# Kernel optimization log

Measured on AMD Instinct MI355X. Metric: run time of the kernel, lower is better.

The kernel has to match this reference:

```python
import jax, jax.numpy as jnp
import numpy as np

B, D, C_IN = 2, 64, 4
N1, N2, N3, N4 = 32, 64, 96, 128
MQ, K = 1024, 5
DN = ('NCDHW', 'OIDHW', 'NCDHW')
PAD = [(2, 2)] * 3  # centered 5^3 kernel, matches Minkowski offsets in [-2, 2]


def setup_inputs() -> dict:
    rng = np.random.default_rng(0)
    mask = rng.random((B, D, D, D)) < 0.2
    x_feat = (rng.standard_normal((B, C_IN, D, D, D)) * mask[:, None]).astype(np.float32)
    Q_F = rng.random((B, MQ, 2)).astype(np.float32)  # per-point quality features (2 channels)

    def conv(cin, cout):
        w = (rng.standard_normal((cout, cin, K, K, K)) / np.sqrt(cin * K ** 3)).astype(np.float32)
        b = (0.01 * rng.standard_normal(cout)).astype(np.float32)
        return w, b

    def gdn(c):
        beta = np.ones(c, np.float32)
        gamma = (1e-4 * rng.random((c, c, K, K, K))).astype(np.float32)
        gamma[np.arange(c), np.arange(c), K // 2, K // 2, K // 2] += 0.1
        return beta, gamma

    w1, b1 = conv(C_IN, N1)
    w2, b2 = conv(N1, N2)
    w3, b3 = conv(N2, N3)
    w4, b4 = conv(N3, N4)
    beta1, gamma1 = gdn(N1)
    beta2, gamma2 = gdn(N2)
    beta3, gamma3 = gdn(N3)
    out = dict(x_feat=x_feat, mask=mask, Q_F=Q_F,
               w1=w1, b1=b1, w2=w2, b2=b2, w3=w3, b3=b3, w4=w4, b4=b4,
               beta1=beta1, gamma1=gamma1, beta2=beta2, gamma2=gamma2,
               beta3=beta3, gamma3=gamma3)
    return {k: jnp.asarray(v) for k, v in out.items()}


def _conv3d(x, w, b, stride):
    y = jax.lax.conv_general_dilated(x, w, (stride,) * 3, PAD, dimension_numbers=DN)
    return y + b[None, :, None, None, None]


def _pool_mask(m):
    # Minkowski stride-2 output coords = any occupied input in each 2x2x2 cell
    b, d = m.shape[0], m.shape[1]
    return m.reshape(b, d // 2, 2, d // 2, 2, d // 2, 2).max(axis=(2, 4, 6))


def _gdn(x, beta, gamma, scale, m):
    # conditional GDN: y = x / sqrt(beta + conv5(gamma, x^2)), scaled per batch by q[:,0]
    den = jax.lax.conv_general_dilated(x * x, gamma, (1, 1, 1), PAD, dimension_numbers=DN)
    y = x * jax.lax.rsqrt(beta[None, :, None, None, None] + den)
    return y * scale * m[:, None]


def reference(x_feat, mask, Q_F, w1, b1, w2, b2, w3, b3, w4, b4,
              beta1, gamma1, beta2, gamma2, beta3, gamma3):
    m0 = mask.astype(x_feat.dtype)
    q = jnp.mean(Q_F, axis=1)[None]                       # [1, B, 2]: per-batch mean of Q.F
    scale = q[0, :, 0][:, None, None, None, None]         # per-batch conditional scale

    c0 = m0.sum(axis=(1, 2, 3))                           # count_per_batch(x)
    m1 = _pool_mask(m0)
    x = _gdn(_conv3d(x_feat, w1, b1, 2) * m1[:, None], beta1, gamma1, scale, m1)
    c1 = m1.sum(axis=(1, 2, 3))
    m2 = _pool_mask(m1)
    x = _gdn(_conv3d(x, w2, b2, 2) * m2[:, None], beta2, gamma2, scale, m2)
    c2 = m2.sum(axis=(1, 2, 3))
    m3 = _pool_mask(m2)
    x = _gdn(_conv3d(x, w3, b3, 2) * m3[:, None], beta3, gamma3, scale, m3)
    x = _conv3d(x, w4, b4, 1) * m3[:, None]               # stride-1 conv keeps coords
    k = jnp.stack([c2, c1, c0]).astype(jnp.int32)         # k.reverse() in the original
    return x, q, k
```

## Files before the change

### kernel.cpp

```cpp
#include <hip/hip_runtime.h>
#include <math.h>

constexpr int Bn  = 2;
constexpr int CIN = 4;
constexpr int MQn = 1024;
constexpr int D0 = 64, D1 = 32, D2 = 16, D3 = 8;

constexpr int OUT_X = 0;
constexpr int OUT_Q = 131072;
constexpr int OUT_K = 131076;

constexpr size_t OFF_CNT   = 0;
constexpr size_t OFF_ZERO  = 8;
constexpr size_t OFF_D1    = 16;
constexpr size_t OFF_T2    = OFF_D1 + 2097152;
constexpr size_t OFF_D2    = OFF_T2 + 524288;
constexpr size_t OFF_T3    = OFF_D2 + 524288;
constexpr size_t OFF_D3    = OFF_T3 + 98304;
constexpr size_t ZERO_END  = OFF_D3 + 98304;
constexpr size_t OFF_SCALE = 3342360;
constexpr size_t OFF_M1    = 3342368;
constexpr size_t OFF_M2    = OFF_M1 + 65536;
constexpr size_t OFF_M3    = OFF_M2 + 8192;
constexpr size_t OFF_T1    = OFF_M3 + 1024;
constexpr size_t OFF_Y1    = OFF_T1 + 2097152;
constexpr size_t OFF_Y2    = OFF_Y1 + 2097152;
constexpr size_t OFF_SQ1   = OFF_Y2 + 524288;
constexpr size_t OFF_SQ2   = OFF_SQ1 + 1048576;
constexpr size_t OFF_SQ3   = OFF_SQ2 + 262144;
constexpr size_t OFF_Y3C   = OFF_SQ3 + 49152;
constexpr size_t OFF_W1T   = OFF_Y3C + 49152;
constexpr size_t OFF_W2T   = OFF_W1T + 16000;
constexpr size_t OFF_W3T   = OFF_W2T + 256000;
constexpr size_t OFF_WB1   = OFF_W3T + 768000;
constexpr size_t OFF_WB2   = OFF_WB1 + 64000;
constexpr size_t OFF_WB3   = OFF_WB2 + 256000;
constexpr size_t OFF_WB4   = OFF_WB3 + 576000;
constexpr size_t OFF_PU    = 12248736;
constexpr size_t OFF_Y1HL  = OFF_PU + 9437184;
constexpr size_t OFF_WB2S  = OFF_Y1HL + 3145728;
constexpr size_t OFF_WB1S  = OFF_WB2S + 384000;
constexpr size_t OFF_WB3S  = OFF_WB1S + 32000;
constexpr size_t OFF_Y2HL  = OFF_WB3S + 1152000;

typedef float v4f __attribute__((ext_vector_type(4)));
typedef __attribute__((ext_vector_type(8)))  short bf16x8v;
typedef __attribute__((ext_vector_type(4)))  short bf16x4v;
typedef __attribute__((ext_vector_type(16))) float f32x16v;

__device__ __forceinline__ void async_copy16(const float* g, float* l) {
    __builtin_amdgcn_global_load_lds(
        (const __attribute__((address_space(1))) void*)g,
        (__attribute__((address_space(3))) void*)l, 16, 0, 0);
}
__device__ __forceinline__ unsigned short f2bf(float f) {
    unsigned u = __float_as_uint(f);
    return (unsigned short)((u + 0x7FFFu + ((u >> 16) & 1u)) >> 16);
}
__device__ __forceinline__ float bf2f(unsigned short h) {
    return __uint_as_float((unsigned)h << 16);
}

__global__ void qmean_kernel(const float* __restrict__ QF, float* __restrict__ out_q,
                             float* __restrict__ scale) {
    int b = blockIdx.x >> 1, c = blockIdx.x & 1;
    float s = 0.f;
    for (int m = threadIdx.x; m < MQn; m += blockDim.x)
        s += QF[(b * MQn + m) * 2 + c];
    __shared__ float sh[256];
    sh[threadIdx.x] = s;
    __syncthreads();
    for (int st = 128; st > 0; st >>= 1) {
        if (threadIdx.x < st) sh[threadIdx.x] += sh[threadIdx.x + st];
        __syncthreads();
    }
    if (threadIdx.x == 0) {
        float mean = sh[0] / (float)MQn;
        out_q[b * 2 + c] = mean;
        if (c == 0) scale[b] = mean;
    }
}

__global__ void mask_pool1_kernel(const float* __restrict__ xf, float* __restrict__ m1,
                                  float* __restrict__ c0) {
    int idx = blockIdx.x * blockDim.x + threadIdx.x;
    int b = idx >> 15;
    int v = idx & 32767;
    int oz = v >> 10, oy = (v >> 5) & 31, ox = v & 31;
    float cnt = 0.f, mx = 0.f;
    for (int dz = 0; dz < 2; ++dz)
        for (int dy = 0; dy < 2; ++dy)
            for (int dx = 0; dx < 2; ++dx) {
                int z = 2 * oz + dz, y = 2 * oy + dy, x = 2 * ox + dx;
                size_t base = (size_t)b * CIN * D0 * D0 * D0 + ((size_t)z * D0 + y) * D0 + x;
                bool occ = false;
                for (int c = 0; c < CIN; ++c)
                    occ = occ || (xf[base + (size_t)c * D0 * D0 * D0] != 0.f);
                if (occ) { cnt += 1.f; mx = 1.f; }
            }
    m1[idx] = mx;
    __shared__ float sh[256];
    sh[threadIdx.x] = cnt;
    __syncthreads();
    for (int st = 128; st > 0; st >>= 1) {
        if (threadIdx.x < st) sh[threadIdx.x] += sh[threadIdx.x + st];
        __syncthreads();
    }
    if (threadIdx.x == 0) atomicAdd(&c0[b], sh[0]);
}

__global__ void pool_kernel(const float* __restrict__ min_, float* __restrict__ mout,
                            float* __restrict__ cacc, int Din) {
    int Do = Din >> 1;
    int per = Do * Do * Do;
    int idx = blockIdx.x * blockDim.x + threadIdx.x;
    int b = idx / per;
    int v = idx % per;
    int oz = v / (Do * Do), oy = (v / Do) % Do, ox = v % Do;
    float s = 0.f, mx = 0.f;
    for (int dz = 0; dz < 2; ++dz)
        for (int dy = 0; dy < 2; ++dy)
            for (int dx = 0; dx < 2; ++dx) {
                float val = min_[(((size_t)b * Din + 2 * oz + dz) * Din + 2 * oy + dy) * Din + 2 * ox + dx];
                s += val;
                mx = fmaxf(mx, val);
            }
    mout[idx] = mx;
    __shared__ float sh[256];
    sh[threadIdx.x] = s;
    __syncthreads();
    for (int st = 128; st > 0; st >>= 1) {
        if (threadIdx.x < st) sh[threadIdx.x] += sh[threadIdx.x + st];
        __syncthreads();
    }
    if (threadIdx.x == 0) atomicAdd(&cacc[b], sh[0]);
}

__global__ void writek_kernel(const float* __restrict__ cnt, float* __restrict__ outk) {
    int i = threadIdx.x;
    if (i < 6) {
        int row = i >> 1, b = i & 1;
        float v = (row == 0) ? cnt[4 + b] : (row == 1 ? cnt[2 + b] : cnt[b]);
        outk[i] = v;
    }
}

constexpr int MS1 = 0,        ME1 = 128000;
constexpr int MS2 = 128000,   ME2 = 640000;
constexpr int MS3 = 640000,   ME3 = 1792000;
constexpr int MS4 = 1792000,  ME4 = 3328000;
__global__ __launch_bounds__(256) void mwtrans_all_kernel(
        const float* __restrict__ g1, const float* __restrict__ g2,
        const float* __restrict__ g3, const float* __restrict__ w4,
        float* __restrict__ ws) {
    int idx = blockIdx.x * 256 + threadIdx.x;
    if (idx >= ME4) return;
    const float* src; unsigned short* dst; int nchn, cin, o;
    if (idx < ME1)      { src = g1; dst = (unsigned short*)(ws + OFF_WB1); nchn = 1; cin = 32; o = idx - MS1; }
    else if (idx < ME2) { src = g2; dst = (unsigned short*)(ws + OFF_WB2); nchn = 2; cin = 64; o = idx - MS2; }
    else if (idx < ME3) { src = g3; dst = (unsigned short*)(ws + OFF_WB3); nchn = 3; cin = 96; o = idx - MS3; }
    else                { src = w4; dst = (unsigned short*)(ws + OFF_WB4); nchn = 4; cin = 96; o = idx - MS4; }
    int j  = o & 7;
    int kc = (o >> 3) & 1;
    int n  = (o >> 4) & 31;
    int q  = o >> 9;
    int tap = q % 125;
    int q2  = q / 125;
    int nch = q2 % nchn;
    int cs  = q2 / nchn;
    int co = nch * 32 + n;
    int ci = cs * 16 + kc * 8 + j;
    dst[o] = f2bf(src[((size_t)co * cin + ci) * 125 + tap]);
}

constexpr int W2S_N = 768000;
__global__ __launch_bounds__(256) void w2s_kernel(const float* __restrict__ w2,
        unsigned short* __restrict__ dst) {
    int o = blockIdx.x * 256 + threadIdx.x;
    if (o >= W2S_N) return;
    int j = o & 7; int kc = (o >> 3) & 1; int n = (o >> 4) & 31; int q = o >> 9;
    int tap = q % 125; int q2 = q / 125; int c = q2 & 1; int cs = q2 >> 1;
    int co = c * 32 + n;
    int e = cs * 16 + kc * 8 + j;
    int ci = e & 31;
    float wv = w2[((size_t)co * 32 + ci) * 125 + tap];
    unsigned short h = f2bf(wv);
    if (e >= 64) h = f2bf(wv - bf2f(h));
    dst[o] = h;
}

constexpr int W3S_N = 2304000;
__global__ __launch_bounds__(256) void w3s_kernel(const float* __restrict__ w3,
        unsigned short* __restrict__ dst) {
    int o = blockIdx.x * 256 + threadIdx.x;
    if (o >= W3S_N) return;
    int j = o & 7; int kc = (o >> 3) & 1; int n = (o >> 4) & 31; int q = o >> 9;
    int tap = q % 125; int q2 = q / 125; int nch = q2 % 3; int cs = q2 / 3;
    int co = nch * 32 + n;
    int e = cs * 16 + kc * 8 + j;
    int ci = e & 63;
    float wv = w3[((size_t)co * 64 + ci) * 125 + tap];
    unsigned short h = f2bf(wv);
    if (e >= 128) h = f2bf(wv - bf2f(h));
    dst[o] = h;
}

constexpr int W1S_N = 64000;
__global__ __launch_bounds__(256) void w1s_kernel(const float* __restrict__ w1,
        unsigned short* __restrict__ dst) {
    int o = blockIdx.x * 256 + threadIdx.x;
    if (o >= W1S_N) return;
    int j = o & 7; int kc = (o >> 3) & 1; int n = (o >> 4) & 31; int tap = o >> 9;
    int ci = j & 3;
    unsigned short h;
    float wv = w1[((size_t)n * 4 + ci) * 125 + tap];
    unsigned short hi = f2bf(wv);
    if (kc == 0)       h = hi;
    else if (j < 4)    h = f2bf(wv - bf2f(hi));
    else               h = 0;
    dst[o] = h;
}

__global__ __launch_bounds__(256) void xcl_kernel(const float* __restrict__ xf,
        unsigned short* __restrict__ xcl) {
    int idx = blockIdx.x * 256 + threadIdx.x;
    int s = idx & 262143; int b = idx >> 18;
    bf16x8v o;
#pragma unroll
    for (int ci = 0; ci < 4; ++ci) {
        float f = xf[((size_t)(b * 4 + ci) << 18) + s];
        unsigned short h = f2bf(f);
        o[ci] = (short)h;
        o[4 + ci] = (short)f2bf(f - bf2f(h));
    }
    *(bf16x8v*)(xcl + (size_t)idx * 8) = o;
}

__global__ __launch_bounds__(256) void mconv1_s2_kernel(
    const unsigned short* __restrict__ xcl,
    const unsigned short* __restrict__ wb,
    const float* __restrict__ bias, const float* __restrict__ mask,
    const float* __restrict__ zerow,
    float* __restrict__ t1, unsigned short* __restrict__ sqcl)
{
    constexpr int DIN = 64, DOUT = 32;
    constexpr int NTX = 4, NTY = 8;
    int r = blockIdx.x;
    int tx0 = (r % NTX) * 8; r /= NTX;
    int ty0 = (r % NTY) * 4; r /= NTY;
    int tz0 = (r % 8) * 4;   int b = r / 8;

    int tid = threadIdx.x;
    int lane = tid & 63, w = tid >> 6;
    int n = lane & 31, kc = lane >> 5;
    int oz = tz0 + w, oy = ty0 + (n >> 3), ox = tx0 + (n & 7);

    f32x16v acc;
#pragma unroll
    for (int i = 0; i < 16; ++i) acc[i] = 0.f;

#pragma unroll 1
    for (int kz = 0; kz < 5; ++kz) {
        int gz = 2 * oz + kz - 2;
        bool zok = (unsigned)gz < (unsigned)DIN;
#pragma unroll 1
        for (int ky = 0; ky < 5; ++ky) {
            int gy = 2 * oy + ky - 2;
            bool zyok = zok && ((unsigned)gy < (unsigned)DIN);
            long long rowbase = (((long long)(b * DIN + gz) * DIN + gy) * DIN) * 8;
#pragma unroll
            for (int kx = 0; kx < 5; ++kx) {
                int gx = 2 * ox + kx - 2;
                bool ok = zyok && ((unsigned)gx < (unsigned)DIN);
                const unsigned short* g = ok ? xcl + (rowbase + (long long)gx * 8)
                                             : (const unsigned short*)zerow;
                bf16x8v dfrag = *(const bf16x8v*)g;
                int tap = (kz * 5 + ky) * 5 + kx;
                const unsigned short* wp = wb + ((size_t)tap << 9) + n * 16 + kc * 8;
                bf16x8v wfrag = *(const bf16x8v*)wp;
                acc = __builtin_amdgcn_mfma_f32_32x32x16_bf16(wfrag, dfrag, acc, 0, 0, 0);
            }
        }
    }

    int sp = (oz * DOUT + oy) * DOUT + ox;
    float mval = mask[b * DOUT * DOUT * DOUT + sp];
#pragma unroll
    for (int q = 0; q < 4; ++q) {
        int co0 = 8 * q + 4 * kc;
        bf16x4v s4;
#pragma unroll
        for (int j = 0; j < 4; ++j) {
            int co = co0 + j;
            float v = (acc[4 * q + j] + bias[co]) * mval;
            t1[(size_t)(b * 32 + co) * 32768 + sp] = v;
            s4[j] = (short)f2bf(v * v);
        }
        *(bf16x4v*)(sqcl + ((size_t)(b * 32768 + sp)) * 32 + co0) = s4;
    }
}

__global__ __launch_bounds__(128) void gdn_cl1_kernel(const float* __restrict__ t,
        const float* __restrict__ pd, const float* __restrict__ beta,
        const float* __restrict__ scale, unsigned short* __restrict__ yhl) {
    constexpr size_t NTOT = (size_t)Bn * 32 * 32768;
    int idx = blockIdx.x * 128 + threadIdx.x;
    int sp = idx & 32767; int b = idx >> 15;
    float sc = scale[b];
    bf16x8v blk[12];
#pragma unroll
    for (int g = 0; g < 4; ++g) {
#pragma unroll
        for (int j = 0; j < 8; ++j) {
            int ci = g * 8 + j;
            size_t p = (size_t)(b * 32 + ci) * 32768 + sp;
            float den = pd[p] + pd[NTOT + p];
            float v = t[p] * rsqrtf(beta[ci] + den) * sc;
            unsigned short h = f2bf(v);
            blk[g][j] = (short)h;
            blk[4 + g][j] = (short)f2bf(v - bf2f(h));
            blk[8 + g][j] = (short)h;
        }
    }
    unsigned short* o = yhl + (size_t)idx * 96;
#pragma unroll
    for (int g = 0; g < 12; ++g) *(bf16x8v*)(o + g * 8) = blk[g];
}

__global__ __launch_bounds__(128) void gdn_cl2_kernel(const float* __restrict__ t,
        const float* __restrict__ pd, const float* __restrict__ beta,
        const float* __restrict__ scale, unsigned short* __restrict__ yhl) {
    constexpr size_t NTOT = (size_t)Bn * 64 * 4096;
    int idx = blockIdx.x * 128 + threadIdx.x;
    if (idx >= Bn * 4096) return;
    int sp = idx & 4095; int b = idx >> 12;
    float sc = scale[b];
    bf16x8v blk[24];
#pragma unroll
    for (int g = 0; g < 8; ++g) {
#pragma unroll
        for (int j = 0; j < 8; ++j) {
            int ci = g * 8 + j;
            size_t p = (size_t)(b * 64 + ci) * 4096 + sp;
            float den = pd[p] + pd[NTOT + p] + pd[2 * NTOT + p] + pd[3 * NTOT + p];
            float v = t[p] * rsqrtf(beta[ci] + den) * sc;
            unsigned short h = f2bf(v);
            blk[g][j] = (short)h;
            blk[8 + g][j] = (short)f2bf(v - bf2f(h));
            blk[16 + g][j] = (short)h;
        }
    }
    unsigned short* o = yhl + (size_t)idx * 192;
#pragma unroll
    for (int g = 0; g < 24; ++g) *(bf16x8v*)(o + g * 8) = blk[g];
}

template<int CINe, int COUTt, int DIN, int DOUT, int CIG, int ZSPL>
__global__ __launch_bounds__(256) void mconv_s2l_kernel(
    const unsigned short* __restrict__ in,
    const unsigned short* __restrict__ wb,
    const float* __restrict__ zerow,
    float* __restrict__ pout)
{
    constexpr int NCH = COUTt / 32;
    constexpr int NTZ = DOUT / 4, NTY = DOUT / 4, NTX = (DOUT >= 8) ? DOUT / 8 : 1;
    constexpr int NT = NTZ * NTY * NTX * Bn;
    constexpr int VOX = DOUT * DOUT * DOUT;
    constexpr int KZSP = (ZSPL == 5) ? 1 : ((ZSPL == 3) ? 2 : 5);
    constexpr int LZH = 6 + KZSP, LYH = 11, LXH = 19;
    constexpr int HV = LZH * LYH * LXH;
    constexpr int UN = 2 * HV;
    constexpr int NLOAD = (UN + 255) / 256;
    __shared__ unsigned short lds[NLOAD * 256 * 8];

    int tile = blockIdx.x % NT; int rest = blockIdx.x / NT;
    int cs = rest % CIG; int zig = rest / CIG;
    int r = tile;
    int tx0 = (r % NTX) * 8; r /= NTX;
    int ty0 = (r % NTY) * 4; r /= NTY;
    int tz0 = (r % NTZ) * 4; int b = r / NTZ;

    int kzlo, kzhi;
    if (ZSPL == 5)      { kzlo = zig;     kzhi = zig + 1; }
    else if (ZSPL == 3) { kzlo = 2 * zig; kzhi = (2 * zig + 2 < 5) ? 2 * zig + 2 : 5; }
    else                { kzlo = 0;       kzhi = 5; }

    int tid = threadIdx.x;
    int iz0 = 2 * tz0 + kzlo - 2, iy0 = 2 * ty0 - 2, ix0 = 2 * tx0 - 2;
#pragma unroll
    for (int k = 0; k < NLOAD; ++k) {
        int u = tid + k * 256;
        int v = u >> 1, half = u & 1;
        int lx = v % LXH; int t = v / LXH;
        int ly = t % LYH, lz = t / LYH;
        int gz = iz0 + lz, gy = iy0 + ly, gx = ix0 + lx;
        bool valid = (v < HV) &&
                     (unsigned)gz < (unsigned)DIN && (unsigned)gy < (unsigned)DIN &&
                     (unsigned)gx < (unsigned)DIN;
        const unsigned short* g = valid
            ? in + ((((size_t)b * DIN + gz) * DIN + gy) * DIN + gx) * CINe + cs * 16 + half * 8
            : (const unsigned short*)zerow;
        async_copy16((const float*)g, (float*)&lds[(size_t)u * 8]);
    }
    __syncthreads();

    int lane = tid & 63, w = tid >> 6;
    int n = lane & 31, kc = lane >> 5;
    int oz = tz0 + w, oy = ty0 + (n >> 3), ox = tx0 + (n & 7);
    int zb = 2 * w, yb = 2 * (n >> 3), xb = 2 * (n & 7);

    f32x16v acc[NCH];
#pragma unroll
    for (int c = 0; c < NCH; ++c)
#pragma unroll
        for (int i = 0; i < 16; ++i) acc[c][i] = 0.f;

#pragma unroll 1
    for (int kz = kzlo; kz < kzhi; ++kz) {
        int zloc = zb + (kz - kzlo);
#pragma unroll 1
        for (int ky = 0; ky < 5; ++ky) {
            int rowb = (zloc * LYH + yb + ky) * LXH + xb;
#pragma unroll
            for (int kx = 0; kx < 5; ++kx) {
                bf16x8v dfrag = *(const bf16x8v*)&lds[(size_t)(rowb + kx) * 16 + kc * 8];
                int tap = (kz * 5 + ky) * 5 + kx;
#pragma unroll
                for (int c = 0; c < NCH; ++c) {
                    const unsigned short* wp =
                        wb + (((size_t)(cs * NCH + c) * 125 + tap) << 9) + n * 16 + kc * 8;
                    bf16x8v wfrag = *(const bf16x8v*)wp;
                    acc[c] = __builtin_amdgcn_mfma_f32_32x32x16_bf16(wfrag, dfrag, acc[c], 0, 0, 0);
                }
            }
        }
    }

    int sp = (oz * DOUT + oy) * DOUT + ox;
#pragma unroll
    for (int c = 0; c < NCH; ++c) {
#pragma unroll
        for (int rr = 0; rr < 16; ++rr) {
            int co = c * 32 + (rr & 3) + 8 * (rr >> 2) + 4 * kc;
            pout[((size_t)((zig * CIG + cs) * Bn + b) * COUTt + co) * VOX + sp] = acc[c][rr];
        }
    }
}

template<int CINe, int COUTt, int DIN, int DOUT, int CIG, int ZSPL>
__global__ __launch_bounds__(256) void mconv_s2_kernel(
    const unsigned short* __restrict__ in,
    const unsigned short* __restrict__ wb,
    const float* __restrict__ zerow,
    float* __restrict__ pout)
{
    constexpr int NCH = COUTt / 32;
    constexpr int NTZ = DOUT / 4, NTY = DOUT / 4, NTX = (DOUT >= 8) ? DOUT / 8 : 1;
    constexpr int NT = NTZ * NTY * NTX * Bn;
    constexpr int VOX = DOUT * DOUT * DOUT;

    int tile = blockIdx.x % NT; int rest = blockIdx.x / NT;
    int cs = rest % CIG; int zig = rest / CIG;
    int r = tile;
    int tx0 = (r % NTX) * 8; r /= NTX;
    int ty0 = (r % NTY) * 4; r /= NTY;
    int tz0 = (r % NTZ) * 4; int b = r / NTZ;

    int tid = threadIdx.x;
    int lane = tid & 63, w = tid >> 6;
    int n = lane & 31, kc = lane >> 5;
    int oz = tz0 + w, oy = ty0 + (n >> 3), ox = tx0 + (n & 7);

    f32x16v acc[NCH];
#pragma unroll
    for (int c = 0; c < NCH; ++c)
#pragma unroll
        for (int i = 0; i < 16; ++i) acc[c][i] = 0.f;

    int kzlo, kzhi;
    if (ZSPL == 5)      { kzlo = zig;     kzhi = zig + 1; }
    else if (ZSPL == 3) { kzlo = 2 * zig; kzhi = (2 * zig + 2 < 5) ? 2 * zig + 2 : 5; }
    else                { kzlo = 0;       kzhi = 5; }
#pragma unroll 1
    for (int kz = kzlo; kz < kzhi; ++kz) {
        int gz = 2 * oz + kz - 2;
        bool zok = (unsigned)gz < (unsigned)DIN;
#pragma unroll 1
        for (int ky = 0; ky < 5; ++ky) {
            int gy = 2 * oy + ky - 2;
            bool zyok = zok && ((unsigned)gy < (unsigned)DIN);
            long long rowbase = (((long long)(b * DIN + gz) * DIN + gy) * DIN) * CINe
                                + cs * 16 + kc * 8;
#pragma unroll
            for (int kx = 0; kx < 5; ++kx) {
                int gx = 2 * ox + kx - 2;
                bool ok = zyok && ((unsigned)gx < (unsigned)DIN);
                const unsigned short* g = ok ? in + (rowbase + (long long)gx * CINe)
                                             : (const unsigned short*)zerow;
                bf16x8v dfrag = *(const bf16x8v*)g;
                int tap = (kz * 5 + ky) * 5 + kx;
#pragma unroll
                for (int c = 0; c < NCH; ++c) {
                    const unsigned short* wp =
                        wb + (((size_t)(cs * NCH + c) * 125 + tap) << 9) + n * 16 + kc * 8;
                    bf16x8v wfrag = *(const bf16x8v*)wp;
                    acc[c] = __builtin_amdgcn_mfma_f32_32x32x16_bf16(wfrag, dfrag, acc[c], 0, 0, 0);
                }
            }
        }
    }

    int sp = (oz * DOUT + oy) * DOUT + ox;
#pragma unroll
    for (int c = 0; c < NCH; ++c) {
#pragma unroll
        for (int rr = 0; rr < 16; ++rr) {
            int co = c * 32 + (rr & 3) + 8 * (rr >> 2) + 4 * kc;
            pout[((size_t)((zig * CIG + cs) * Bn + b) * COUTt + co) * VOX + sp] = acc[c][rr];
        }
    }
}

template<int CS, int COUTt, int VOX>
__global__ __launch_bounds__(256) void red_epi_kernel(const float* __restrict__ P,
        const float* __restrict__ bias, const float* __restrict__ mask,
        float* __restrict__ buf, unsigned short* __restrict__ sqcl) {
    constexpr int NTOT = Bn * COUTt * VOX;
    int idx = blockIdx.x * 256 + threadIdx.x;
    if (idx >= NTOT) return;
    int sp = idx % VOX;
    int co = (idx / VOX) % COUTt;
    int b = idx / (VOX * COUTt);
    float s = 0.f;
#pragma unroll
    for (int k = 0; k < CS; ++k) s += P[(size_t)k * NTOT + idx];
    float v = (s + bias[co]) * mask[b * VOX + sp];
    buf[idx] = v;
    sqcl[((size_t)b * VOX + sp) * COUTt + co] = f2bf(v * v);
}

template<int CINt, int COUTt, int Dd, int TZ, int YB, int CIG, int ZSPL>
__global__ __launch_bounds__(256) void mconv_kernel(
    const unsigned short* __restrict__ in,
    const unsigned short* __restrict__ wb,
    const float* __restrict__ zerow,
    float* __restrict__ pout)
{
    constexpr int NCH = COUTt / 32;
    constexpr int LZ = TZ + 4, LYH = YB * 4 + 4, LXH = 12;
    constexpr int HV = LZ * LYH * LXH;
    constexpr int UN = 2 * HV;
    constexpr int NLOAD = (UN + 255) / 256;
    constexpr int NTZ = Dd / TZ, NTY = Dd / (YB * 4), NTX = Dd / 8;
    constexpr int NT = NTZ * NTY * NTX * Bn;
    constexpr int VOX = Dd * Dd * Dd;
    __shared__ unsigned short lds[NLOAD * 256 * 8];

    int bid = blockIdx.x;
    int tile = bid % NT; int rest = bid / NT;
    int cs = rest % CIG; int zig = rest / CIG;
    int r = tile;
    int tx0 = (r % NTX) * 8; r /= NTX;
    int ty0 = (r % NTY) * (YB * 4); r /= NTY;
    int tz0 = (r % NTZ) * TZ; int b = r / NTZ;

    int tid = threadIdx.x;
    int iz0 = tz0 - 2, iy0 = ty0 - 2, ix0 = tx0 - 2;
#pragma unroll
    for (int k = 0; k < NLOAD; ++k) {
        int u = tid + k * 256;
        int v = u >> 1, half = u & 1;
        int lx = v % LXH; int t = v / LXH;
        int ly = t % LYH, lz = t / LYH;
        int gz = iz0 + lz, gy = iy0 + ly, gx = ix0 + lx;
        bool valid = (v < HV) &&
                     (unsigned)gz < (unsigned)Dd && (unsigned)gy < (unsigned)Dd &&
                     (unsigned)gx < (unsigned)Dd;
        const unsigned short* g = valid
            ? in + ((((size_t)b * Dd + gz) * Dd + gy) * Dd + gx) * CINt + cs * 16 + half * 8
            : (const unsigned short*)zerow;
        async_copy16((const float*)g, (float*)&lds[(size_t)u * 8]);
    }
    __syncthreads();

    int lane = tid & 63, w = tid >> 6;
    int zz = (YB == 1) ? w : (w >> 1);
    int yb = (YB == 1) ? 0 : (w & 1);
    int n = lane & 31, kc = lane >> 5;
    int vy = yb * 4 + (n >> 3), vx = n & 7;

    f32x16v acc[NCH];
#pragma unroll
    for (int c = 0; c < NCH; ++c)
#pragma unroll
        for (int i = 0; i < 16; ++i) acc[c][i] = 0.f;

    int kzlo = (ZSPL == 5) ? zig : 0;
    int kzhi = (ZSPL == 5) ? zig + 1 : 5;
#pragma unroll 1
    for (int kz = kzlo; kz < kzhi; ++kz) {
#pragma unroll 1
        for (int ky = 0; ky < 5; ++ky) {
            int hvrow = ((zz + kz) * LYH + (vy + ky)) * LXH + vx;
#pragma unroll
            for (int kx = 0; kx < 5; ++kx) {
                bf16x8v dfrag = *(const bf16x8v*)&lds[(size_t)(hvrow + kx) * 16 + kc * 8];
                int tap = (kz * 5 + ky) * 5 + kx;
#pragma unroll
                for (int c = 0; c < NCH; ++c) {
                    const unsigned short* wp =
                        wb + (((size_t)(cs * NCH + c) * 125 + tap) << 9) + n * 16 + kc * 8;
                    bf16x8v wfrag = *(const bf16x8v*)wp;
                    acc[c] = __builtin_amdgcn_mfma_f32_32x32x16_bf16(wfrag, dfrag, acc[c], 0, 0, 0);
                }
            }
        }
    }

    int g = rest;
    int sp = ((tz0 + zz) * Dd + (ty0 + vy)) * Dd + (tx0 + vx);
#pragma unroll
    for (int c = 0; c < NCH; ++c) {
#pragma unroll
        for (int rr = 0; rr < 16; ++rr) {
            int co = c * 32 + (rr & 3) + 8 * (rr >> 2) + 4 * kc;
            pout[((size_t)(g * Bn + b) * COUTt + co) * VOX + sp] = acc[c][rr];
        }
    }
}

template<int G, int COUTt, int DOUT>
__global__ __launch_bounds__(256) void gdn_red_cl_kernel(const float* __restrict__ t,
        const float* __restrict__ pd, const float* __restrict__ beta,
        const float* __restrict__ scale, unsigned short* __restrict__ ycl) {
    constexpr int VOX = DOUT * DOUT * DOUT;
    constexpr int NTOT = Bn * COUTt * VOX;
    int idx = blockIdx.x * 256 + threadIdx.x;
    if (idx >= NTOT) return;
    int sp = idx % VOX;
    int co = (idx / VOX) % COUTt;
    int b = idx / (VOX * COUTt);
    float den = 0.f;
#pragma unroll
    for (int k = 0; k < G; ++k) den += pd[(size_t)k * NTOT + idx];
    float v = t[idx] * rsqrtf(beta[co] + den) * scale[b];
    ycl[((size_t)b * VOX + sp) * COUTt + co] = f2bf(v);
}

template<int G, int COUTt, int DOUT>
__global__ __launch_bounds__(256) void conv_red_kernel(const float* __restrict__ pc,
        const float* __restrict__ bias, const float* __restrict__ mask,
        float* __restrict__ outx) {
    constexpr int VOX = DOUT * DOUT * DOUT;
    constexpr int NTOT = Bn * COUTt * VOX;
    int idx = blockIdx.x * 256 + threadIdx.x;
    if (idx >= NTOT) return;
    int sp = idx % VOX;
    int co = (idx / VOX) % COUTt;
    int b = idx / (VOX * COUTt);
    float s = 0.f;
#pragma unroll
    for (int k = 0; k < G; ++k) s += pc[(size_t)k * NTOT + idx];
    outx[idx] = (s + bias[co]) * mask[b * VOX + sp];
}

extern "C" void kernel_launch(void* const* d_in, const int* in_sizes, int n_in,
                              void* d_out, int out_size, void* d_ws, size_t ws_size,
                              hipStream_t stream) {
    const float* x_feat = (const float*)d_in[0];
    const float* QF     = (const float*)d_in[2];
    const float* w1 = (const float*)d_in[3];  const float* b1 = (const float*)d_in[4];
    const float* w2 = (const float*)d_in[5];  const float* b2 = (const float*)d_in[6];
    const float* w3 = (const float*)d_in[7];  const float* b3 = (const float*)d_in[8];
    const float* w4 = (const float*)d_in[9];  const float* b4 = (const float*)d_in[10];
    const float* beta1 = (const float*)d_in[11]; const float* gamma1 = (const float*)d_in[12];
    const float* beta2 = (const float*)d_in[13]; const float* gamma2 = (const float*)d_in[14];
    const float* beta3 = (const float*)d_in[15]; const float* gamma3 = (const float*)d_in[16];

    float* out = (float*)d_out;
    float* ws = (float*)d_ws;
    float* cnt   = ws + OFF_CNT;
    float* zerow = ws + OFF_ZERO;
    float* scale = ws + OFF_SCALE;
    float* m1 = ws + OFF_M1;  float* m2 = ws + OFF_M2;  float* m3 = ws + OFF_M3;
    float* t1 = ws + OFF_T1;
    float* t2 = ws + OFF_T2;
    float* t3 = ws + OFF_T3;
    float* pu = ws + OFF_PU;
    unsigned short* sq1 = (unsigned short*)(ws + OFF_SQ1);
    unsigned short* sq2 = (unsigned short*)(ws + OFF_SQ2);
    unsigned short* sq3 = (unsigned short*)(ws + OFF_SQ3);
    unsigned short* y3c = (unsigned short*)(ws + OFF_Y3C);
    unsigned short* y1hl = (unsigned short*)(ws + OFF_Y1HL);
    unsigned short* y2hl = (unsigned short*)(ws + OFF_Y2HL);
    unsigned short* xcl = (unsigned short*)(ws + OFF_Y1);
    unsigned short* wb1 = (unsigned short*)(ws + OFF_WB1);
    unsigned short* wb2 = (unsigned short*)(ws + OFF_WB2);
    unsigned short* wb3 = (unsigned short*)(ws + OFF_WB3);
    unsigned short* wb4 = (unsigned short*)(ws + OFF_WB4);
    unsigned short* wb1s = (unsigned short*)(ws + OFF_WB1S);
    unsigned short* wb2s = (unsigned short*)(ws + OFF_WB2S);
    unsigned short* wb3s = (unsigned short*)(ws + OFF_WB3S);

    hipMemsetAsync(ws, 0, 16 * sizeof(float), stream);

    qmean_kernel<<<4, 256, 0, stream>>>(QF, out + OUT_Q, scale);
    mask_pool1_kernel<<<256, 256, 0, stream>>>(x_feat, m1, cnt + 0);
    pool_kernel<<<32, 256, 0, stream>>>(m1, m2, cnt + 2, D1);
    pool_kernel<<<4, 256, 0, stream>>>(m2, m3, cnt + 4, D2);
    writek_kernel<<<1, 64, 0, stream>>>(cnt, out + OUT_K);

    mwtrans_all_kernel<<<(ME4 + 255) / 256, 256, 0, stream>>>(gamma1, gamma2, gamma3, w4, ws);
    w1s_kernel<<<(W1S_N + 255) / 256, 256, 0, stream>>>(w1, wb1s);
    w2s_kernel<<<(W2S_N + 255) / 256, 256, 0, stream>>>(w2, wb2s);
    w3s_kernel<<<(W3S_N + 255) / 256, 256, 0, stream>>>(w3, wb3s);
    xcl_kernel<<<2048, 256, 0, stream>>>(x_feat, xcl);

    mconv1_s2_kernel<<<512, 256, 0, stream>>>(xcl, wb1s, b1, m1, zerow, t1, sq1);
    mconv_kernel<32, 32, 32, 4, 1, 2, 1>
        <<<1024, 256, 0, stream>>>(sq1, wb1, zerow, pu);
    gdn_cl1_kernel<<<512, 128, 0, stream>>>(t1, pu, beta1, scale, y1hl);

    mconv_s2l_kernel<96, 64, 32, 16, 6, 3>
        <<<64 * 6 * 3, 256, 0, stream>>>(y1hl, wb2s, zerow, pu);
    red_epi_kernel<18, 64, 4096><<<2048, 256, 0, stream>>>(pu, b2, m2, t2, sq2);
    mconv_kernel<64, 64, 16, 4, 1, 4, 1>
        <<<256, 256, 0, stream>>>(sq2, wb2, zerow, pu);
    gdn_cl2_kernel<<<64, 128, 0, stream>>>(t2, pu, beta2, scale, y2hl);

    mconv_s2_kernel<192, 96, 16, 8, 12, 5>
        <<<8 * 12 * 5, 256, 0, stream>>>(y2hl, wb3s, zerow, pu);
    red_epi_kernel<60, 96, 512><<<384, 256, 0, stream>>>(pu, b3, m3, t3, sq3);
    mconv_kernel<96, 96, 8, 2, 2, 6, 5>
        <<<240, 256, 0, stream>>>(sq3, wb3, zerow, pu);
    gdn_red_cl_kernel<30, 96, 8><<<384, 256, 0, stream>>>(t3, pu, beta3, scale, y3c);

    mconv_kernel<96, 128, 8, 2, 2, 6, 5>
        <<<240, 256, 0, stream>>>(y3c, wb4, zerow, pu);
    conv_red_kernel<30, 128, 8><<<512, 256, 0, stream>>>(pu, b4, m3, out + OUT_X);
}
```

Measured before the change: 415.4 us.

## Store layer-1 GDN output as split planes and read conv2 input directly from global

The GDN1 kernel now writes hi/lo bf16 values into four separate 16-channel planes instead of one interleaved 96-wide record that duplicated the hi part. Conv2 loses its LDS halo staging and its barrier, and each lane gathers its 16-byte fragment from global memory by plane index. This removes a redundant write of the hi copy and the LDS fill and sync. In exchange, conv2 loads come straight from global or L2 for every tap with bounds checks, which relies on cache reuse across taps.

After: 399.6 us. -3.8%, faster.

```diff
diff --git a/kernel.cpp b/kernel.cpp
--- a/kernel.cpp
+++ b/kernel.cpp
@@ -37,8 +37,8 @@
 constexpr size_t OFF_WB3   = OFF_WB2 + 256000;
 constexpr size_t OFF_WB4   = OFF_WB3 + 576000;
 constexpr size_t OFF_PU    = 12248736;
-constexpr size_t OFF_Y1HL  = OFF_PU + 9437184;
-constexpr size_t OFF_WB2S  = OFF_Y1HL + 3145728;
+constexpr size_t OFF_Y1P   = OFF_PU + 9437184;
+constexpr size_t OFF_WB2S  = OFF_Y1P + 3145728;
 constexpr size_t OFF_WB1S  = OFF_WB2S + 384000;
 constexpr size_t OFF_WB3S  = OFF_WB1S + 32000;
 constexpr size_t OFF_Y2HL  = OFF_WB3S + 1152000;
@@ -302,12 +302,13 @@
 
 __global__ __launch_bounds__(128) void gdn_cl1_kernel(const float* __restrict__ t,
         const float* __restrict__ pd, const float* __restrict__ beta,
-        const float* __restrict__ scale, unsigned short* __restrict__ yhl) {
+        const float* __restrict__ scale, unsigned short* __restrict__ y1p) {
     constexpr size_t NTOT = (size_t)Bn * 32 * 32768;
+    constexpr size_t PLSZ = (size_t)Bn * 32768 * 16;
     int idx = blockIdx.x * 128 + threadIdx.x;
     int sp = idx & 32767; int b = idx >> 15;
     float sc = scale[b];
-    bf16x8v blk[12];
+    bf16x8v hi[4], lo[4];
 #pragma unroll
     for (int g = 0; g < 4; ++g) {
 #pragma unroll
@@ -317,14 +318,19 @@
             float den = pd[p] + pd[NTOT + p];
             float v = t[p] * rsqrtf(beta[ci] + den) * sc;
             unsigned short h = f2bf(v);
-            blk[g][j] = (short)h;
-            blk[4 + g][j] = (short)f2bf(v - bf2f(h));
-            blk[8 + g][j] = (short)h;
-        }
-    }
-    unsigned short* o = yhl + (size_t)idx * 96;
-#pragma unroll
-    for (int g = 0; g < 12; ++g) *(bf16x8v*)(o + g * 8) = blk[g];
+            hi[g][j] = (short)h;
+            lo[g][j] = (short)f2bf(v - bf2f(h));
+        }
+    }
+    size_t vo = ((size_t)b * 32768 + sp) * 16;
+    *(bf16x8v*)(y1p + 0 * PLSZ + vo)     = hi[0];
+    *(bf16x8v*)(y1p + 0 * PLSZ + vo + 8) = hi[1];
+    *(bf16x8v*)(y1p + 1 * PLSZ + vo)     = hi[2];
+    *(bf16x8v*)(y1p + 1 * PLSZ + vo + 8) = hi[3];
+    *(bf16x8v*)(y1p + 2 * PLSZ + vo)     = lo[0];
+    *(bf16x8v*)(y1p + 2 * PLSZ + vo + 8) = lo[1];
+    *(bf16x8v*)(y1p + 3 * PLSZ + vo)     = lo[2];
+    *(bf16x8v*)(y1p + 3 * PLSZ + vo + 8) = lo[3];
 }
 
 __global__ __launch_bounds__(128) void gdn_cl2_kernel(const float* __restrict__ t,
@@ -355,8 +361,8 @@
     for (int g = 0; g < 24; ++g) *(bf16x8v*)(o + g * 8) = blk[g];
 }
 
-template<int CINe, int COUTt, int DIN, int DOUT, int CIG, int ZSPL>
-__global__ __launch_bounds__(256) void mconv_s2l_kernel(
+template<int COUTt, int DIN, int DOUT, int CIG, int ZSPL, int PLN>
+__global__ __launch_bounds__(256) void mconv_s2p_kernel(
     const unsigned short* __restrict__ in,
     const unsigned short* __restrict__ wb,
     const float* __restrict__ zerow,
@@ -366,64 +372,49 @@
     constexpr int NTZ = DOUT / 4, NTY = DOUT / 4, NTX = (DOUT >= 8) ? DOUT / 8 : 1;
     constexpr int NT = NTZ * NTY * NTX * Bn;
     constexpr int VOX = DOUT * DOUT * DOUT;
-    constexpr int KZSP = (ZSPL == 5) ? 1 : ((ZSPL == 3) ? 2 : 5);
-    constexpr int LZH = 6 + KZSP, LYH = 11, LXH = 19;
-    constexpr int HV = LZH * LYH * LXH;
-    constexpr int UN = 2 * HV;
-    constexpr int NLOAD = (UN + 255) / 256;
-    __shared__ unsigned short lds[NLOAD * 256 * 8];
+    constexpr size_t PLSZ = (size_t)Bn * DIN * DIN * DIN * 16;
 
     int tile = blockIdx.x % NT; int rest = blockIdx.x / NT;
     int cs = rest % CIG; int zig = rest / CIG;
+    int pl = cs % PLN;
     int r = tile;
     int tx0 = (r % NTX) * 8; r /= NTX;
     int ty0 = (r % NTY) * 4; r /= NTY;
     int tz0 = (r % NTZ) * 4; int b = r / NTZ;
 
+    int tid = threadIdx.x;
+    int lane = tid & 63, w = tid >> 6;
+    int n = lane & 31, kc = lane >> 5;
+    int oz = tz0 + w, oy = ty0 + (n >> 3), ox = tx0 + (n & 7);
+
+    const unsigned short* inp = in + (size_t)pl * PLSZ;
+
+    f32x16v acc[NCH];
+#pragma unroll
+    for (int c = 0; c < NCH; ++c)
+#pragma unroll
+        for (int i = 0; i < 16; ++i) acc[c][i] = 0.f;
+
     int kzlo, kzhi;
     if (ZSPL == 5)      { kzlo = zig;     kzhi = zig + 1; }
     else if (ZSPL == 3) { kzlo = 2 * zig; kzhi = (2 * zig + 2 < 5) ? 2 * zig + 2 : 5; }
     else                { kzlo = 0;       kzhi = 5; }
-
-    int tid = threadIdx.x;
-    int iz0 = 2 * tz0 + kzlo - 2, iy0 = 2 * ty0 - 2, ix0 = 2 * tx0 - 2;
-#pragma unroll
-    for (int k = 0; k < NLOAD; ++k) {
-        int u = tid + k * 256;
-        int v = u >> 1, half = u & 1;
-        int lx = v % LXH; int t = v / LXH;
-        int ly = t % LYH, lz = t / LYH;
-        int gz = iz0 + lz, gy = iy0 + ly, gx = ix0 + lx;
-        bool valid = (v < HV) &&
-                     (unsigned)gz < (unsigned)DIN && (unsigned)gy < (unsigned)DIN &&
-                     (unsigned)gx < (unsigned)DIN;
-        const unsigned short* g = valid
-            ? in + ((((size_t)b * DIN + gz) * DIN + gy) * DIN + gx) * CINe + cs * 16 + half * 8
-            : (const unsigned short*)zerow;
-        async_copy16((const float*)g, (float*)&lds[(size_t)u * 8]);
-    }
-    __syncthreads();
-
-    int lane = tid & 63, w = tid >> 6;
-    int n = lane & 31, kc = lane >> 5;
-    int oz = tz0 + w, oy = ty0 + (n >> 3), ox = tx0 + (n & 7);
-    int zb = 2 * w, yb = 2 * (n >> 3), xb = 2 * (n & 7);
-
-    f32x16v acc[NCH];
-#pragma unroll
-    for (int c = 0; c < NCH; ++c)
-#pragma unroll
-        for (int i = 0; i < 16; ++i) acc[c][i] = 0.f;
-
 #pragma unroll 1
     for (int kz = kzlo; kz < kzhi; ++kz) {
-        int zloc = zb + (kz - kzlo);
+        int gz = 2 * oz + kz - 2;
+        bool zok = (unsigned)gz < (unsigned)DIN;
 #pragma unroll 1
         for (int ky = 0; ky < 5; ++ky) {
-            int rowb = (zloc * LYH + yb + ky) * LXH + xb;
+            int gy = 2 * oy + ky - 2;
+            bool zyok = zok && ((unsigned)gy < (unsigned)DIN);
+            long long rowbase = (((long long)(b * DIN + gz) * DIN + gy) * DIN) * 16 + kc * 8;
 #pragma unroll
             for (int kx = 0; kx < 5; ++kx) {
-                bf16x8v dfrag = *(const bf16x8v*)&lds[(size_t)(rowb + kx) * 16 + kc * 8];
+                int gx = 2 * ox + kx - 2;
+                bool ok = zyok && ((unsigned)gx < (unsigned)DIN);
+                const unsigned short* g = ok ? inp + (rowbase + (long long)gx * 16)
+                                             : (const unsigned short*)zerow;
+                bf16x8v dfrag = *(const bf16x8v*)g;
                 int tap = (kz * 5 + ky) * 5 + kx;
 #pragma unroll
                 for (int c = 0; c < NCH; ++c) {
@@ -691,7 +682,7 @@
     unsigned short* sq2 = (unsigned short*)(ws + OFF_SQ2);
     unsigned short* sq3 = (unsigned short*)(ws + OFF_SQ3);
     unsigned short* y3c = (unsigned short*)(ws + OFF_Y3C);
-    unsigned short* y1hl = (unsigned short*)(ws + OFF_Y1HL);
+    unsigned short* y1p = (unsigned short*)(ws + OFF_Y1P);
     unsigned short* y2hl = (unsigned short*)(ws + OFF_Y2HL);
     unsigned short* xcl = (unsigned short*)(ws + OFF_Y1);
     unsigned short* wb1 = (unsigned short*)(ws + OFF_WB1);
@@ -719,10 +710,10 @@
     mconv1_s2_kernel<<<512, 256, 0, stream>>>(xcl, wb1s, b1, m1, zerow, t1, sq1);
     mconv_kernel<32, 32, 32, 4, 1, 2, 1>
         <<<1024, 256, 0, stream>>>(sq1, wb1, zerow, pu);
-    gdn_cl1_kernel<<<512, 128, 0, stream>>>(t1, pu, beta1, scale, y1hl);
-
-    mconv_s2l_kernel<96, 64, 32, 16, 6, 3>
-        <<<64 * 6 * 3, 256, 0, stream>>>(y1hl, wb2s, zerow, pu);
+    gdn_cl1_kernel<<<512, 128, 0, stream>>>(t1, pu, beta1, scale, y1p);
+
+    mconv_s2p_kernel<64, 32, 16, 6, 3, 4>
+        <<<64 * 6 * 3, 256, 0, stream>>>(y1p, wb2s, zerow, pu);
     red_epi_kernel<18, 64, 4096><<<2048, 256, 0, stream>>>(pu, b2, m2, t2, sq2);
     mconv_kernel<64, 64, 16, 4, 1, 4, 1>
         <<<256, 256, 0, stream>>>(sq2, wb2, zerow, pu);
```
